# Kernel optimization log

Measured on AMD Instinct MI355X. Metric: run time of the kernel, lower is better.

Reference implementation:

```python
import jax, jax.numpy as jnp
import numpy as np
import math

B, C, A, W, H = 8, 128, 16, 64, 64


def setup_inputs() -> dict:
    key = jax.random.key(0)
    ks = jax.random.split(key, 7)
    s_in = 1.0 / math.sqrt(C)
    return {
        "x": jax.random.normal(ks[0], (B, C, W, H), dtype=jnp.float32),
        "Wq": jax.random.normal(ks[1], (A, C), dtype=jnp.float32) * s_in,
        "bq": jnp.zeros((A,), dtype=jnp.float32),
        "Wk": jax.random.normal(ks[2], (A, C), dtype=jnp.float32) * s_in,
        "bk": jnp.zeros((A,), dtype=jnp.float32),
        "Wv": jax.random.normal(ks[3], (C, C), dtype=jnp.float32) * s_in,
        "bv": jnp.zeros((C,), dtype=jnp.float32),
    }


def reference(x, Wq, bq, Wk, bk, Wv, bv):
    # 1x1 convs == per-pixel linear projections
    q = jnp.einsum('ac,bcwh->bawh', Wq, x) + bq[None, :, None, None]  # [B,A,W,H]
    k = jnp.einsum('ac,bcwh->bawh', Wk, x) + bk[None, :, None, None]  # [B,A,W,H]
    v = jnp.einsum('vc,bcwh->bvwh', Wv, x) + bv[None, :, None, None]  # [B,C,W,H]

    scale = 1.0 / math.sqrt(q.shape[1])
    # full spatial attention: [B, W, H, W, H]
    attn = jnp.einsum('bawh,baWH->bwhWH', q, k)
    b, w, h, _, _ = attn.shape
    attn = jax.nn.softmax(attn.reshape(b, w, h, -1) * scale, axis=-1)
    attn = attn.reshape(b, w, h, w, h)
    out = jnp.einsum('bwhWH,bvWH->bvwh', attn, v)  # [B,C,W,H]
    return out
```

## Files before the change

### kernel.cpp

```cpp
#include <hip/hip_runtime.h>
#include <math.h>

#define BB 8
#define CC 128
#define NN 4096

typedef _Float16 f16;
typedef _Float16 f16x4v __attribute__((ext_vector_type(4)));
typedef _Float16 f16x8 __attribute__((ext_vector_type(8)));
typedef float f32x4v __attribute__((ext_vector_type(4)));
typedef float f32x16 __attribute__((ext_vector_type(16)));

#if __has_builtin(__builtin_amdgcn_exp2f)
#define EXP2(x) __builtin_amdgcn_exp2f(x)
#else
#define EXP2(x) __expf((x)*0.69314718056f)
#endif

#define QSCALE 0.360673760222f
#define SHIFT  5.770780163555f

#define WF_BYTES 65536

__global__ __launch_bounds__(256)
void prep_kernel(const float* __restrict__ Wq, const float* __restrict__ bq,
                 const float* __restrict__ Wk, const float* __restrict__ bk,
                 const float* __restrict__ Wv, const float* __restrict__ bv,
                 f16* __restrict__ Wf, float* __restrict__ biasS)
{
    const int tg = blockIdx.x*256 + threadIdx.x;
    if (tg < 2560) {
        const int mt = tg >> 9, ks = (tg >> 6) & 7, l = tg & 63;
        const int n32 = l & 31, h = l >> 5;
        const int r = mt*32 + n32;
        f16x8 v8;
        #pragma unroll
        for (int i = 0; i < 8; i++) {
            int c = ks*16 + 8*h + i;
            float wv_;
            if (r < 16)      wv_ = QSCALE * Wq[r*CC + c];
            else if (r < 32) wv_ = Wk[(r-16)*CC + c];
            else             wv_ = Wv[(r-32)*CC + c];
            v8[i] = (f16)wv_;
        }
        *(f16x8*)&Wf[(size_t)tg*8] = v8;
    }
    if (blockIdx.x == 0 && threadIdx.x < 160) {
        int r = threadIdx.x;
        biasS[r] = r < 16 ? QSCALE*bq[r] : (r < 32 ? bk[r-16] : bv[r-32]);
    }
}

__global__ __launch_bounds__(256)
void proj_kernel(const float* __restrict__ x, const f16* __restrict__ Wf,
                 const float* __restrict__ biasS,
                 f16* __restrict__ Qt, f16* __restrict__ Kt, f16* __restrict__ Vf)
{
    __shared__ __align__(16) f16 Vl[CC*140];

    const int tid  = threadIdx.x;
    const int lane = tid & 63;
    const int wv   = tid >> 6;
    const int b    = blockIdx.x & 7;
    const int pt   = blockIdx.x >> 3;
    const int n32  = lane & 31;
    const int half = lane >> 5;
    const int p    = pt*128 + wv*32 + n32;

    const float* xp = x + (size_t)b*CC*NN + p;
    f16x8 xf[8];
    #pragma unroll
    for (int ks = 0; ks < 8; ks++) {
        float xv[8];
        #pragma unroll
        for (int i = 0; i < 8; i++)
            xv[i] = __builtin_nontemporal_load(&xp[(size_t)(ks*16 + 8*half + i)*NN]);
        #pragma unroll
        for (int i = 0; i < 8; i++) xf[ks][i] = (f16)xv[i];
    }

    f32x16 acc[5];
    #pragma unroll
    for (int mt = 0; mt < 5; mt++) acc[mt] = (f32x16)0.0f;
    #pragma unroll
    for (int ks = 0; ks < 8; ks++) {
        #pragma unroll
        for (int mt = 0; mt < 5; mt++) {
            f16x8 wfr = *(const f16x8*)&Wf[((size_t)(mt*8 + ks)*64 + lane)*8];
            acc[mt] = __builtin_amdgcn_mfma_f32_32x32x16_f16(wfr, xf[ks], acc[mt], 0, 0, 0);
        }
    }

    #pragma unroll
    for (int mt = 0; mt < 5; mt++) {
        #pragma unroll
        for (int q = 0; q < 4; q++) {
            float4 b4 = *(const float4*)&biasS[mt*32 + q*8 + 4*half];
            acc[mt][q*4+0] += b4.x; acc[mt][q*4+1] += b4.y;
            acc[mt][q*4+2] += b4.z; acc[mt][q*4+3] += b4.w;
        }
    }

    {
        size_t qkoff = ((size_t)b*NN + p)*16;
        f16x4v s0, s1, s2, s3;
        #pragma unroll
        for (int i = 0; i < 4; i++) {
            s0[i] = (f16)acc[0][i];    s1[i] = (f16)acc[0][4+i];
            s2[i] = (f16)acc[0][8+i];  s3[i] = (f16)acc[0][12+i];
        }
        *(f16x4v*)&Qt[qkoff + 4*half]     = s0;
        *(f16x4v*)&Qt[qkoff + 8 + 4*half] = s1;
        *(f16x4v*)&Kt[qkoff + 4*half]     = s2;
        *(f16x4v*)&Kt[qkoff + 8 + 4*half] = s3;
    }

    #pragma unroll
    for (int mt = 1; mt < 5; mt++) {
        #pragma unroll
        for (int g = 0; g < 16; g++) {
            int c = (mt-1)*32 + (g & 3) + 8*(g >> 2) + 4*half;
            Vl[c*140 + wv*32 + n32] = (f16)acc[mt][g];
        }
    }
    __syncthreads();

    #pragma unroll
    for (int pass = 0; pass < 8; pass++) {
        int item = pass*256 + tid;
        int l    = item & 63;
        int f    = (item >> 6) & 15;
        int ktl  = item >> 10;
        int c16  = f >> 2, ct = f & 3;
        int li   = l & 31, h2 = l >> 5;
        const f16* src = &Vl[(ct*32 + li)*140 + ktl*64 + c16*16 + 4*h2];
        f16x4v lo = *(const f16x4v*)&src[0];
        f16x4v hi = *(const f16x4v*)&src[8];
        f16x8 v8;
        #pragma unroll
        for (int i = 0; i < 4; i++) { v8[i] = lo[i]; v8[4+i] = hi[i]; }
        int ktg = pt*2 + ktl;
        *(f16x8*)&Vf[((((size_t)b*64 + ktg)*16 + c16*4 + ct)*64 + l)*8] = v8;
    }
}

__global__ __launch_bounds__(256, 2)
void attn_kernel(const f16* __restrict__ Qt, const f16* __restrict__ Kt,
                 const f16* __restrict__ Vf, float* __restrict__ out)
{
    __shared__ __align__(16) unsigned char lds_raw[27776];

    const int tid  = threadIdx.x;
    const int lane = tid & 63;
    const int wv   = tid >> 6;
    const int b    = blockIdx.x & 7;
    const int qt   = blockIdx.x >> 3;
    const int q0   = qt*32;
    const int n32  = lane & 31;
    const int half = lane >> 5;

    const f16* vb = Vf + (size_t)b*64*16*512;
    const f16* kb = Kt + (size_t)b*NN*16;
    const f16x8 qf = *(const f16x8*)&Qt[((size_t)b*NN + q0 + n32)*16 + half*8];

    f32x16 of[4];
    #pragma unroll
    for (int ct = 0; ct < 4; ct++) of[ct] = (f32x16)0.0f;
    float ps[4] = {0.f, 0.f, 0.f, 0.f};

    f16x8 kf0 = *(const f16x8*)&kb[((size_t)wv*64 + n32)*16 + half*8];
    f16x8 kf1 = *(const f16x8*)&kb[((size_t)wv*64 + 32 + n32)*16 + half*8];
    f16x8 vpf[16];
    {
        const f16* vt = vb + (size_t)wv*8192;
        #pragma unroll
        for (int i = 0; i < 16; i++)
            vpf[i] = *(const f16x8*)&vt[((size_t)i*64 + lane)*8];
    }

    for (int kt = wv; kt < NN/64; kt += 4) {
        const int ktn = (kt + 4 < NN/64) ? kt + 4 : kt;
        f16x8 kf0n = *(const f16x8*)&kb[((size_t)ktn*64 + n32)*16 + half*8];
        f16x8 kf1n = *(const f16x8*)&kb[((size_t)ktn*64 + 32 + n32)*16 + half*8];

        f32x16 St0 = __builtin_amdgcn_mfma_f32_32x32x16_f16(kf0, qf, (f32x16)(-SHIFT), 0, 0, 0);
        f32x16 St1 = __builtin_amdgcn_mfma_f32_32x32x16_f16(kf1, qf, (f32x16)(-SHIFT), 0, 0, 0);

        f16x8 pf[4];
        #pragma unroll
        for (int g = 0; g < 16; g++) {
            float e0 = EXP2(St0[g]); ps[g & 3] += e0; pf[(g >> 3)][g & 7]     = (f16)e0;
            float e1 = EXP2(St1[g]); ps[g & 3] += e1; pf[2 + (g >> 3)][g & 7] = (f16)e1;
        }

        const f16* vtn = vb + (size_t)ktn*8192;
        #pragma unroll
        for (int kc = 0; kc < 4; kc++) {
            #pragma unroll
            for (int ct = 0; ct < 4; ct++) {
                const int i = kc*4 + ct;
                f16x8 vc = vpf[i];
                vpf[i] = *(const f16x8*)&vtn[((size_t)i*64 + lane)*8];
                of[ct] = __builtin_amdgcn_mfma_f32_32x32x16_f16(pf[kc], vc, of[ct], 0, 0, 0);
            }
        }
        kf0 = kf0n; kf1 = kf1n;
    }

    float ls = (ps[0] + ps[1]) + (ps[2] + ps[3]);
    ls += __shfl_xor(ls, 32);

    __syncthreads();
    if (wv != 0) {
        unsigned char* base = lds_raw + (size_t)(wv-1)*9216 + (size_t)lane*144;
        #pragma unroll
        for (int ct = 0; ct < 4; ct++) {
            #pragma unroll
            for (int h = 0; h < 2; h++) {
                f16x8 t;
                #pragma unroll
                for (int jj = 0; jj < 8; jj++) t[jj] = (f16)of[ct][h*8+jj];
                *(f16x8*)(base + ct*32 + h*16) = t;
            }
        }
        *(float*)(base + 128) = ls;
    }
    __syncthreads();
    if (wv == 0) {
        #pragma unroll
        for (int s2 = 0; s2 < 3; s2++) {
            unsigned char* base = lds_raw + (size_t)s2*9216 + (size_t)lane*144;
            #pragma unroll
            for (int ct = 0; ct < 4; ct++) {
                #pragma unroll
                for (int h = 0; h < 2; h++) {
                    f16x8 t = *(const f16x8*)(base + ct*32 + h*16);
                    #pragma unroll
                    for (int jj = 0; jj < 8; jj++) of[ct][h*8+jj] += (float)t[jj];
                }
            }
            ls += *(const float*)(base + 128);
        }
        float* ls_inv = (float*)(lds_raw + 27648);
        if (lane < 32) ls_inv[lane] = 1.f / ls;
        float invq[16];
        #pragma unroll
        for (int g = 0; g < 16; g++)
            invq[g] = ls_inv[(g & 3) + 8*(g >> 2) + 4*half];
        float* Tb = (float*)lds_raw;
        #pragma unroll
        for (int ct = 0; ct < 4; ct++) {
            #pragma unroll
            for (int g = 0; g < 16; g++) {
                int row = (g & 3) + 8*(g >> 2) + 4*half;
                Tb[(ct*32 + n32)*36 + row] = of[ct][g] * invq[g];
            }
        }
    }
    __syncthreads();
    {
        const float* Tb = (const float*)lds_raw;
        #pragma unroll
        for (int it = 0; it < 4; it++) {
            int idx = it*256 + tid;
            int c = idx >> 3, qq = idx & 7;
            f32x4v v = *(const f32x4v*)&Tb[c*36 + qq*4];
            __builtin_nontemporal_store(v,
                (f32x4v*)&out[((size_t)b*CC + c)*NN + q0 + qq*4]);
        }
    }
}

extern "C" void kernel_launch(void* const* d_in, const int* in_sizes, int n_in,
                              void* d_out, int out_size, void* d_ws, size_t ws_size,
                              hipStream_t stream) {
    const float* x  = (const float*)d_in[0];
    const float* Wq = (const float*)d_in[1];
    const float* bq = (const float*)d_in[2];
    const float* Wk = (const float*)d_in[3];
    const float* bk = (const float*)d_in[4];
    const float* Wv = (const float*)d_in[5];
    const float* bv = (const float*)d_in[6];
    float* out = (float*)d_out;

    f16* Qw = (f16*)d_ws;
    f16* Kw = Qw + (size_t)BB*NN*16;
    f16* Vw = Kw + (size_t)BB*NN*16;
    unsigned char* tail = (unsigned char*)d_out + (size_t)out_size*4 - WF_BYTES;
    f16*   Wf    = (f16*)tail;
    float* biasS = (float*)(tail + 49152);

    hipLaunchKernelGGL(prep_kernel, dim3(10), dim3(256), 0, stream,
                       Wq, bq, Wk, bk, Wv, bv, Wf, biasS);
    hipLaunchKernelGGL(proj_kernel, dim3(256), dim3(256), 0, stream,
                       x, Wf, biasS, Qw, Kw, Vw);
    hipLaunchKernelGGL(attn_kernel, dim3(1024), dim3(256), 0, stream,
                       Qw, Kw, Vw, out);
}
```

Baseline: 136.7 us.

## Process 64 queries per block with waves split over channel pairs and key halves

```diff
diff --git a/kernel.cpp b/kernel.cpp
--- a/kernel.cpp
+++ b/kernel.cpp
@@ -148,125 +148,163 @@
 void attn_kernel(const f16* __restrict__ Qt, const f16* __restrict__ Kt,
                  const f16* __restrict__ Vf, float* __restrict__ out)
 {
-    __shared__ __align__(16) unsigned char lds_raw[27776];
+    __shared__ __align__(16) unsigned char lds_raw[53504];
 
     const int tid  = threadIdx.x;
     const int lane = tid & 63;
     const int wv   = tid >> 6;
+    const int cp   = wv & 1;
+    const int kh   = wv >> 1;
     const int b    = blockIdx.x & 7;
     const int qt   = blockIdx.x >> 3;
-    const int q0   = qt*32;
+    const int q0   = qt*64;
     const int n32  = lane & 31;
     const int half = lane >> 5;
 
     const f16* vb = Vf + (size_t)b*64*16*512;
     const f16* kb = Kt + (size_t)b*NN*16;
-    const f16x8 qf = *(const f16x8*)&Qt[((size_t)b*NN + q0 + n32)*16 + half*8];
-
-    f32x16 of[4];
-    #pragma unroll
-    for (int ct = 0; ct < 4; ct++) of[ct] = (f32x16)0.0f;
-    float ps[4] = {0.f, 0.f, 0.f, 0.f};
-
-    f16x8 kf0 = *(const f16x8*)&kb[((size_t)wv*64 + n32)*16 + half*8];
-    f16x8 kf1 = *(const f16x8*)&kb[((size_t)wv*64 + 32 + n32)*16 + half*8];
-    f16x8 vpf[16];
+    const f16x8 qfA = *(const f16x8*)&Qt[((size_t)b*NN + q0 + n32)*16 + half*8];
+    const f16x8 qfB = *(const f16x8*)&Qt[((size_t)b*NN + q0 + 32 + n32)*16 + half*8];
+
+    f32x16 ofA[2], ofB[2];
+    #pragma unroll
+    for (int c = 0; c < 2; c++) { ofA[c] = (f32x16)0.0f; ofB[c] = (f32x16)0.0f; }
+    float psA[4] = {0.f, 0.f, 0.f, 0.f};
+    float psB[4] = {0.f, 0.f, 0.f, 0.f};
+
+    f16x8 kf0 = *(const f16x8*)&kb[((size_t)kh*64 + n32)*16 + half*8];
+    f16x8 kf1 = *(const f16x8*)&kb[((size_t)kh*64 + 32 + n32)*16 + half*8];
+    f16x8 vpf[8];
     {
-        const f16* vt = vb + (size_t)wv*8192;
-        #pragma unroll
-        for (int i = 0; i < 16; i++)
-            vpf[i] = *(const f16x8*)&vt[((size_t)i*64 + lane)*8];
-    }
-
-    for (int kt = wv; kt < NN/64; kt += 4) {
-        const int ktn = (kt + 4 < NN/64) ? kt + 4 : kt;
+        const f16* vt = vb + (size_t)kh*8192;
+        #pragma unroll
+        for (int kc = 0; kc < 4; kc++)
+            #pragma unroll
+            for (int j = 0; j < 2; j++)
+                vpf[kc*2+j] = *(const f16x8*)&vt[((size_t)(kc*4 + 2*cp + j)*64 + lane)*8];
+    }
+
+    for (int kt = kh; kt < NN/64; kt += 2) {
+        const int ktn = (kt + 2 < NN/64) ? kt + 2 : kt;
         f16x8 kf0n = *(const f16x8*)&kb[((size_t)ktn*64 + n32)*16 + half*8];
         f16x8 kf1n = *(const f16x8*)&kb[((size_t)ktn*64 + 32 + n32)*16 + half*8];
 
-        f32x16 St0 = __builtin_amdgcn_mfma_f32_32x32x16_f16(kf0, qf, (f32x16)(-SHIFT), 0, 0, 0);
-        f32x16 St1 = __builtin_amdgcn_mfma_f32_32x32x16_f16(kf1, qf, (f32x16)(-SHIFT), 0, 0, 0);
-
-        f16x8 pf[4];
-        #pragma unroll
-        for (int g = 0; g < 16; g++) {
-            float e0 = EXP2(St0[g]); ps[g & 3] += e0; pf[(g >> 3)][g & 7]     = (f16)e0;
-            float e1 = EXP2(St1[g]); ps[g & 3] += e1; pf[2 + (g >> 3)][g & 7] = (f16)e1;
+        f16x8 pfA[4];
+        {
+            f32x16 St0 = __builtin_amdgcn_mfma_f32_32x32x16_f16(kf0, qfA, (f32x16)(-SHIFT), 0, 0, 0);
+            f32x16 St1 = __builtin_amdgcn_mfma_f32_32x32x16_f16(kf1, qfA, (f32x16)(-SHIFT), 0, 0, 0);
+            #pragma unroll
+            for (int g = 0; g < 16; g++) {
+                float e0 = EXP2(St0[g]); psA[g & 3] += e0; pfA[(g >> 3)][g & 7]     = (f16)e0;
+                float e1 = EXP2(St1[g]); psA[g & 3] += e1; pfA[2 + (g >> 3)][g & 7] = (f16)e1;
+            }
+        }
+        f16x8 pfB[4];
+        {
+            f32x16 St0 = __builtin_amdgcn_mfma_f32_32x32x16_f16(kf0, qfB, (f32x16)(-SHIFT), 0, 0, 0);
+            f32x16 St1 = __builtin_amdgcn_mfma_f32_32x32x16_f16(kf1, qfB, (f32x16)(-SHIFT), 0, 0, 0);
+            #pragma unroll
+            for (int g = 0; g < 16; g++) {
+                float e0 = EXP2(St0[g]); psB[g & 3] += e0; pfB[(g >> 3)][g & 7]     = (f16)e0;
+                float e1 = EXP2(St1[g]); psB[g & 3] += e1; pfB[2 + (g >> 3)][g & 7] = (f16)e1;
+            }
         }
 
         const f16* vtn = vb + (size_t)ktn*8192;
         #pragma unroll
         for (int kc = 0; kc < 4; kc++) {
             #pragma unroll
-            for (int ct = 0; ct < 4; ct++) {
-                const int i = kc*4 + ct;
-                f16x8 vc = vpf[i];
-                vpf[i] = *(const f16x8*)&vtn[((size_t)i*64 + lane)*8];
-                of[ct] = __builtin_amdgcn_mfma_f32_32x32x16_f16(pf[kc], vc, of[ct], 0, 0, 0);
+            for (int j = 0; j < 2; j++) {
+                const int ii = kc*2 + j;
+                f16x8 vc = vpf[ii];
+                vpf[ii] = *(const f16x8*)&vtn[((size_t)(kc*4 + 2*cp + j)*64 + lane)*8];
+                ofA[j] = __builtin_amdgcn_mfma_f32_32x32x16_f16(pfA[kc], vc, ofA[j], 0, 0, 0);
+                ofB[j] = __builtin_amdgcn_mfma_f32_32x32x16_f16(pfB[kc], vc, ofB[j], 0, 0, 0);
             }
         }
         kf0 = kf0n; kf1 = kf1n;
     }
 
-    float ls = (ps[0] + ps[1]) + (ps[2] + ps[3]);
-    ls += __shfl_xor(ls, 32);
-
-    __syncthreads();
-    if (wv != 0) {
-        unsigned char* base = lds_raw + (size_t)(wv-1)*9216 + (size_t)lane*144;
-        #pragma unroll
-        for (int ct = 0; ct < 4; ct++) {
+    float lsA = (psA[0] + psA[1]) + (psA[2] + psA[3]);
+    lsA += __shfl_xor(lsA, 32);
+    float lsB = (psB[0] + psB[1]) + (psB[2] + psB[3]);
+    lsB += __shfl_xor(lsB, 32);
+
+    __syncthreads();
+    if (wv >= 2) {
+        unsigned char* base = lds_raw + (size_t)cp*9216 + (size_t)lane*144;
+        #pragma unroll
+        for (int a = 0; a < 4; a++) {
             #pragma unroll
             for (int h = 0; h < 2; h++) {
                 f16x8 t;
                 #pragma unroll
-                for (int jj = 0; jj < 8; jj++) t[jj] = (f16)of[ct][h*8+jj];
-                *(f16x8*)(base + ct*32 + h*16) = t;
-            }
-        }
-        *(float*)(base + 128) = ls;
-    }
-    __syncthreads();
-    if (wv == 0) {
-        #pragma unroll
-        for (int s2 = 0; s2 < 3; s2++) {
-            unsigned char* base = lds_raw + (size_t)s2*9216 + (size_t)lane*144;
-            #pragma unroll
-            for (int ct = 0; ct < 4; ct++) {
+                for (int jj = 0; jj < 8; jj++)
+                    t[jj] = (f16)((a < 2 ? ofA[a & 1] : ofB[a & 1])[h*8 + jj]);
+                *(f16x8*)(base + a*32 + h*16) = t;
+            }
+        }
+        *(float*)(base + 128) = lsA;
+        *(float*)(base + 132) = lsB;
+    }
+    __syncthreads();
+    if (wv < 2) {
+        unsigned char* base = lds_raw + (size_t)cp*9216 + (size_t)lane*144;
+        #pragma unroll
+        for (int a = 0; a < 4; a++) {
+            #pragma unroll
+            for (int h = 0; h < 2; h++) {
+                f16x8 t = *(const f16x8*)(base + a*32 + h*16);
                 #pragma unroll
-                for (int h = 0; h < 2; h++) {
-                    f16x8 t = *(const f16x8*)(base + ct*32 + h*16);
+                for (int jj = 0; jj < 8; jj++) {
+                    float v = (float)t[jj];
+                    if (a < 2) ofA[a & 1][h*8 + jj] += v;
+                    else       ofB[a & 1][h*8 + jj] += v;
+                }
+            }
+        }
+        if (wv == 0) {
+            float lsA2 = *(const float*)(base + 128);
+            float lsB2 = *(const float*)(base + 132);
+            float* ls_inv = (float*)(lds_raw + 18432);
+            if (lane < 32) {
+                ls_inv[n32]      = 1.f / (lsA + lsA2);
+                ls_inv[32 + n32] = 1.f / (lsB + lsB2);
+            }
+        }
+    }
+    __syncthreads();
+
+    if (wv < 2) {
+        const float* ls_inv = (const float*)(lds_raw + 18432);
+        float* Tb = (float*)(lds_raw + 18688);
+        #pragma unroll
+        for (int qts = 0; qts < 2; qts++) {
+            #pragma unroll
+            for (int j = 0; j < 4; j++) {
+                f32x4v iv = *(const f32x4v*)&ls_inv[qts*32 + 8*j + 4*half];
+                #pragma unroll
+                for (int ctl = 0; ctl < 2; ctl++) {
+                    const int c = (2*cp + ctl)*32 + n32;
+                    f32x4v o;
                     #pragma unroll
-                    for (int jj = 0; jj < 8; jj++) of[ct][h*8+jj] += (float)t[jj];
+                    for (int e = 0; e < 4; e++)
+                        o[e] = (qts ? ofB[ctl] : ofA[ctl])[4*j + e] * iv[e];
+                    *(f32x4v*)&Tb[(size_t)c*68 + qts*32 + 8*j + 4*half] = o;
                 }
             }
-            ls += *(const float*)(base + 128);
-        }
-        float* ls_inv = (float*)(lds_raw + 27648);
-        if (lane < 32) ls_inv[lane] = 1.f / ls;
-        float invq[16];
-        #pragma unroll
-        for (int g = 0; g < 16; g++)
-            invq[g] = ls_inv[(g & 3) + 8*(g >> 2) + 4*half];
-        float* Tb = (float*)lds_raw;
-        #pragma unroll
-        for (int ct = 0; ct < 4; ct++) {
-            #pragma unroll
-            for (int g = 0; g < 16; g++) {
-                int row = (g & 3) + 8*(g >> 2) + 4*half;
-                Tb[(ct*32 + n32)*36 + row] = of[ct][g] * invq[g];
-            }
         }
     }
     __syncthreads();
     {
-        const float* Tb = (const float*)lds_raw;
-        #pragma unroll
-        for (int it = 0; it < 4; it++) {
+        const float* Tb = (const float*)(lds_raw + 18688);
+        #pragma unroll
+        for (int it = 0; it < 8; it++) {
             int idx = it*256 + tid;
-            int c = idx >> 3, qq = idx & 7;
-            f32x4v v = *(const f32x4v*)&Tb[c*36 + qq*4];
+            int c = idx >> 4, qg = idx & 15;
+            f32x4v v = *(const f32x4v*)&Tb[(size_t)c*68 + qg*4];
             __builtin_nontemporal_store(v,
-                (f32x4v*)&out[((size_t)b*CC + c)*NN + q0 + qq*4]);
+                (f32x4v*)&out[((size_t)b*CC + c)*NN + q0 + qg*4]);
         }
     }
 }
@@ -294,6 +332,6 @@
                        Wq, bq, Wk, bk, Wv, bv, Wf, biasS);
     hipLaunchKernelGGL(proj_kernel, dim3(256), dim3(256), 0, stream,
                        x, Wf, biasS, Qw, Kw, Vw);
-    hipLaunchKernelGGL(attn_kernel, dim3(1024), dim3(256), 0, stream,
+    hipLaunchKernelGGL(attn_kernel, dim3(512), dim3(256), 0, stream,
                        Qw, Kw, Vw, out);
 }
```

Result: no change. 139.1 us (+1.7%).

## Split attention work across waves by channel tile with LDS-shared probabilities

Applied to the files above, without the earlier changes.

```diff
diff --git a/kernel.cpp b/kernel.cpp
--- a/kernel.cpp
+++ b/kernel.cpp
@@ -6,15 +6,26 @@
 #define NN 4096
 
 typedef _Float16 f16;
+typedef _Float16 f16x2 __attribute__((ext_vector_type(2)));
 typedef _Float16 f16x4v __attribute__((ext_vector_type(4)));
 typedef _Float16 f16x8 __attribute__((ext_vector_type(8)));
 typedef float f32x4v __attribute__((ext_vector_type(4)));
 typedef float f32x16 __attribute__((ext_vector_type(16)));
+typedef int i32x4 __attribute__((ext_vector_type(4)));
 
 #if __has_builtin(__builtin_amdgcn_exp2f)
 #define EXP2(x) __builtin_amdgcn_exp2f(x)
 #else
 #define EXP2(x) __expf((x)*0.69314718056f)
+#endif
+
+#if __has_builtin(__builtin_amdgcn_cvt_pkrtz) && __has_builtin(__builtin_amdgcn_fdot2)
+#define CVTPK(a,b)    __builtin_amdgcn_cvt_pkrtz((a),(b))
+#define FDOT2(pk,acc) __builtin_amdgcn_fdot2((pk), one2_, (acc), false)
+#else
+static __device__ inline f16x2 cvtpk_fb(float a, float b){ f16x2 r; r[0]=(f16)a; r[1]=(f16)b; return r; }
+#define CVTPK(a,b)    cvtpk_fb((a),(b))
+#define FDOT2(pk,acc) ((acc) + (float)(pk)[0] + (float)(pk)[1])
 #endif
 
 #define QSCALE 0.360673760222f
@@ -144,130 +155,129 @@
     }
 }
 
-__global__ __launch_bounds__(256, 2)
+__global__ __launch_bounds__(256, 4)
 void attn_kernel(const f16* __restrict__ Qt, const f16* __restrict__ Kt,
                  const f16* __restrict__ Vf, float* __restrict__ out)
 {
-    __shared__ __align__(16) unsigned char lds_raw[27776];
+    __shared__ __align__(16) unsigned char lds_raw[19072];
 
     const int tid  = threadIdx.x;
     const int lane = tid & 63;
-    const int wv   = tid >> 6;
+    const int w    = tid >> 6;
     const int b    = blockIdx.x & 7;
     const int qt   = blockIdx.x >> 3;
     const int q0   = qt*32;
     const int n32  = lane & 31;
     const int half = lane >> 5;
+    const int myhalf = w & 1;
+    const int mypar  = w >> 1;
 
     const f16* vb = Vf + (size_t)b*64*16*512;
     const f16* kb = Kt + (size_t)b*NN*16;
     const f16x8 qf = *(const f16x8*)&Qt[((size_t)b*NN + q0 + n32)*16 + half*8];
 
-    f32x16 of[4];
-    #pragma unroll
-    for (int ct = 0; ct < 4; ct++) of[ct] = (f32x16)0.0f;
-    float ps[4] = {0.f, 0.f, 0.f, 0.f};
-
-    f16x8 kf0 = *(const f16x8*)&kb[((size_t)wv*64 + n32)*16 + half*8];
-    f16x8 kf1 = *(const f16x8*)&kb[((size_t)wv*64 + 32 + n32)*16 + half*8];
-    f16x8 vpf[16];
+    f16* Pex = (f16*)lds_raw;
+    const auto one2_ = CVTPK(1.0f, 1.0f);
+
+    f32x16 of = (f32x16)0.0f;
+    float ls = 0.0f;
+
+    f16x8 kf = *(const f16x8*)&kb[((size_t)(mypar*64 + myhalf*32 + n32))*16 + half*8];
+    f16x8 vpf[4];
+    #pragma unroll
+    for (int kc = 0; kc < 4; kc++)
+        vpf[kc] = *(const f16x8*)&vb[((size_t)(kc*4 + w)*64 + lane)*8];
+
+#define PROD(ST, PAR)                                                          \
+    {                                                                          \
+        i32x4 lo_, hi_;                                                        \
+        _Pragma("unroll")                                                      \
+        for (int e = 0; e < 8; e++) {                                          \
+            float ea_ = EXP2((ST)[2*e]);                                       \
+            float eb_ = EXP2((ST)[2*e+1]);                                     \
+            auto pk_ = CVTPK(ea_, eb_);                                        \
+            ls = FDOT2(pk_, ls);                                               \
+            if (e < 4) lo_[e]   = __builtin_bit_cast(int, pk_);                \
+            else       hi_[e-4] = __builtin_bit_cast(int, pk_);                \
+        }                                                                      \
+        f16* wr_ = &Pex[((size_t)((PAR)*4 + 2*myhalf)*64 + lane)*8];           \
+        *(i32x4*)&wr_[0]   = lo_;                                              \
+        *(i32x4*)&wr_[512] = hi_;                                              \
+    }
+
+    for (int kt2 = 0; kt2 < 64; kt2 += 2) {
+        if (w < 2) {
+            f32x16 St = __builtin_amdgcn_mfma_f32_32x32x16_f16(kf, qf, (f32x16)(-SHIFT), 0, 0, 0);
+            {
+                const int tn = (kt2 + 2 < 64) ? kt2 + 2 : kt2;
+                kf = *(const f16x8*)&kb[((size_t)(tn*64 + myhalf*32 + n32))*16 + half*8];
+            }
+            PROD(St, 0)
+        }
+        asm volatile("s_waitcnt lgkmcnt(0)\n\ts_barrier" ::: "memory");
+        {
+            const f16* vtn = vb + (size_t)(kt2 + 1)*8192;
+            #pragma unroll
+            for (int kc = 0; kc < 4; kc++) {
+                f16x8 pq = *(const f16x8*)&Pex[((size_t)kc*64 + lane)*8];
+                f16x8 vc = vpf[kc];
+                vpf[kc] = *(const f16x8*)&vtn[((size_t)(kc*4 + w)*64 + lane)*8];
+                of = __builtin_amdgcn_mfma_f32_32x32x16_f16(pq, vc, of, 0, 0, 0);
+            }
+        }
+        if (w >= 2) {
+            f32x16 St = __builtin_amdgcn_mfma_f32_32x32x16_f16(kf, qf, (f32x16)(-SHIFT), 0, 0, 0);
+            {
+                const int tn = (kt2 + 3 < 64) ? kt2 + 3 : kt2 + 1;
+                kf = *(const f16x8*)&kb[((size_t)(tn*64 + myhalf*32 + n32))*16 + half*8];
+            }
+            PROD(St, 1)
+        }
+        asm volatile("s_waitcnt lgkmcnt(0)\n\ts_barrier" ::: "memory");
+        {
+            const int tv = (kt2 + 2 < 64) ? kt2 + 2 : 63;
+            const f16* vtn = vb + (size_t)tv*8192;
+            #pragma unroll
+            for (int kc = 0; kc < 4; kc++) {
+                f16x8 pq = *(const f16x8*)&Pex[((size_t)(4 + kc)*64 + lane)*8];
+                f16x8 vc = vpf[kc];
+                vpf[kc] = *(const f16x8*)&vtn[((size_t)(kc*4 + w)*64 + lane)*8];
+                of = __builtin_amdgcn_mfma_f32_32x32x16_f16(pq, vc, of, 0, 0, 0);
+            }
+        }
+    }
+#undef PROD
+
+    float ls2 = ls + __shfl_xor(ls, 32);
+    __syncthreads();
+    float* ls_part = (float*)(lds_raw + 18432);
+    float* ls_inv  = (float*)(lds_raw + 18944);
+    if (lane < 32) ls_part[w*32 + n32] = ls2;
+    __syncthreads();
+    if (w == 0 && lane < 32)
+        ls_inv[n32] = 1.0f / (ls_part[n32] + ls_part[32 + n32] +
+                              ls_part[64 + n32] + ls_part[96 + n32]);
+    __syncthreads();
+    float* Tb = (float*)lds_raw;
     {
-        const f16* vt = vb + (size_t)wv*8192;
-        #pragma unroll
-        for (int i = 0; i < 16; i++)
-            vpf[i] = *(const f16x8*)&vt[((size_t)i*64 + lane)*8];
-    }
-
-    for (int kt = wv; kt < NN/64; kt += 4) {
-        const int ktn = (kt + 4 < NN/64) ? kt + 4 : kt;
-        f16x8 kf0n = *(const f16x8*)&kb[((size_t)ktn*64 + n32)*16 + half*8];
-        f16x8 kf1n = *(const f16x8*)&kb[((size_t)ktn*64 + 32 + n32)*16 + half*8];
-
-        f32x16 St0 = __builtin_amdgcn_mfma_f32_32x32x16_f16(kf0, qf, (f32x16)(-SHIFT), 0, 0, 0);
-        f32x16 St1 = __builtin_amdgcn_mfma_f32_32x32x16_f16(kf1, qf, (f32x16)(-SHIFT), 0, 0, 0);
-
-        f16x8 pf[4];
+        f32x4v iv[4];
+        #pragma unroll
+        for (int t = 0; t < 4; t++)
+            iv[t] = *(const f32x4v*)&ls_inv[t*8 + 4*half];
         #pragma unroll
         for (int g = 0; g < 16; g++) {
-            float e0 = EXP2(St0[g]); ps[g & 3] += e0; pf[(g >> 3)][g & 7]     = (f16)e0;
-            float e1 = EXP2(St1[g]); ps[g & 3] += e1; pf[2 + (g >> 3)][g & 7] = (f16)e1;
-        }
-
-        const f16* vtn = vb + (size_t)ktn*8192;
-        #pragma unroll
-        for (int kc = 0; kc < 4; kc++) {
-            #pragma unroll
-            for (int ct = 0; ct < 4; ct++) {
-                const int i = kc*4 + ct;
-                f16x8 vc = vpf[i];
-                vpf[i] = *(const f16x8*)&vtn[((size_t)i*64 + lane)*8];
-                of[ct] = __builtin_amdgcn_mfma_f32_32x32x16_f16(pf[kc], vc, of[ct], 0, 0, 0);
-            }
-        }
-        kf0 = kf0n; kf1 = kf1n;
-    }
-
-    float ls = (ps[0] + ps[1]) + (ps[2] + ps[3]);
-    ls += __shfl_xor(ls, 32);
-
-    __syncthreads();
-    if (wv != 0) {
-        unsigned char* base = lds_raw + (size_t)(wv-1)*9216 + (size_t)lane*144;
-        #pragma unroll
-        for (int ct = 0; ct < 4; ct++) {
-            #pragma unroll
-            for (int h = 0; h < 2; h++) {
-                f16x8 t;
-                #pragma unroll
-                for (int jj = 0; jj < 8; jj++) t[jj] = (f16)of[ct][h*8+jj];
-                *(f16x8*)(base + ct*32 + h*16) = t;
-            }
-        }
-        *(float*)(base + 128) = ls;
-    }
-    __syncthreads();
-    if (wv == 0) {
-        #pragma unroll
-        for (int s2 = 0; s2 < 3; s2++) {
-            unsigned char* base = lds_raw + (size_t)s2*9216 + (size_t)lane*144;
-            #pragma unroll
-            for (int ct = 0; ct < 4; ct++) {
-                #pragma unroll
-                for (int h = 0; h < 2; h++) {
-                    f16x8 t = *(const f16x8*)(base + ct*32 + h*16);
-                    #pragma unroll
-                    for (int jj = 0; jj < 8; jj++) of[ct][h*8+jj] += (float)t[jj];
-                }
-            }
-            ls += *(const float*)(base + 128);
-        }
-        float* ls_inv = (float*)(lds_raw + 27648);
-        if (lane < 32) ls_inv[lane] = 1.f / ls;
-        float invq[16];
-        #pragma unroll
-        for (int g = 0; g < 16; g++)
-            invq[g] = ls_inv[(g & 3) + 8*(g >> 2) + 4*half];
-        float* Tb = (float*)lds_raw;
-        #pragma unroll
-        for (int ct = 0; ct < 4; ct++) {
-            #pragma unroll
-            for (int g = 0; g < 16; g++) {
-                int row = (g & 3) + 8*(g >> 2) + 4*half;
-                Tb[(ct*32 + n32)*36 + row] = of[ct][g] * invq[g];
-            }
-        }
-    }
-    __syncthreads();
-    {
-        const float* Tb = (const float*)lds_raw;
-        #pragma unroll
-        for (int it = 0; it < 4; it++) {
-            int idx = it*256 + tid;
-            int c = idx >> 3, qq = idx & 7;
-            f32x4v v = *(const f32x4v*)&Tb[c*36 + qq*4];
-            __builtin_nontemporal_store(v,
-                (f32x4v*)&out[((size_t)b*CC + c)*NN + q0 + qq*4]);
-        }
+            int row = (g & 3) + 8*(g >> 2) + 4*half;
+            Tb[(size_t)(w*32 + n32)*36 + row] = of[g] * iv[g >> 2][g & 3];
+        }
+    }
+    __syncthreads();
+    #pragma unroll
+    for (int it = 0; it < 4; it++) {
+        int idx = it*256 + tid;
+        int c = idx >> 3, qg = idx & 7;
+        f32x4v v = *(const f32x4v*)&Tb[(size_t)c*36 + qg*4];
+        __builtin_nontemporal_store(v,
+            (f32x4v*)&out[((size_t)b*CC + c)*NN + q0 + qg*4]);
     }
 }
 
```

Measured after the change: 144.6 us. 5.8% more time.

## Share LDS-staged V tiles across waves with 64-query blocks and split channels

Applied to the files above, without the earlier changes.

```diff
diff --git a/kernel.cpp b/kernel.cpp
--- a/kernel.cpp
+++ b/kernel.cpp
@@ -148,112 +148,111 @@
 void attn_kernel(const f16* __restrict__ Qt, const f16* __restrict__ Kt,
                  const f16* __restrict__ Vf, float* __restrict__ out)
 {
-    __shared__ __align__(16) unsigned char lds_raw[27776];
+    __shared__ __align__(16) unsigned char lds_raw[65536];
 
     const int tid  = threadIdx.x;
     const int lane = tid & 63;
-    const int wv   = tid >> 6;
+    const int w    = tid >> 6;
+    const int qp   = w & 1;
+    const int pw   = w >> 1;
     const int b    = blockIdx.x & 7;
     const int qt   = blockIdx.x >> 3;
-    const int q0   = qt*32;
+    const int q0   = qt*64;
     const int n32  = lane & 31;
     const int half = lane >> 5;
 
     const f16* vb = Vf + (size_t)b*64*16*512;
     const f16* kb = Kt + (size_t)b*NN*16;
-    const f16x8 qf = *(const f16x8*)&Qt[((size_t)b*NN + q0 + n32)*16 + half*8];
-
-    f32x16 of[4];
-    #pragma unroll
-    for (int ct = 0; ct < 4; ct++) of[ct] = (f32x16)0.0f;
+    const f16x8 qf = *(const f16x8*)&Qt[((size_t)b*NN + q0 + qp*32 + n32)*16 + half*8];
+
+    f32x16 of0 = (f32x16)0.0f, of1 = (f32x16)0.0f;
     float ps[4] = {0.f, 0.f, 0.f, 0.f};
 
-    f16x8 kf0 = *(const f16x8*)&kb[((size_t)wv*64 + n32)*16 + half*8];
-    f16x8 kf1 = *(const f16x8*)&kb[((size_t)wv*64 + 32 + n32)*16 + half*8];
-    f16x8 vpf[16];
-    {
-        const f16* vt = vb + (size_t)wv*8192;
-        #pragma unroll
-        for (int i = 0; i < 16; i++)
-            vpf[i] = *(const f16x8*)&vt[((size_t)i*64 + lane)*8];
-    }
-
-    for (int kt = wv; kt < NN/64; kt += 4) {
-        const int ktn = (kt + 4 < NN/64) ? kt + 4 : kt;
-        f16x8 kf0n = *(const f16x8*)&kb[((size_t)ktn*64 + n32)*16 + half*8];
-        f16x8 kf1n = *(const f16x8*)&kb[((size_t)ktn*64 + 32 + n32)*16 + half*8];
-
-        f32x16 St0 = __builtin_amdgcn_mfma_f32_32x32x16_f16(kf0, qf, (f32x16)(-SHIFT), 0, 0, 0);
-        f32x16 St1 = __builtin_amdgcn_mfma_f32_32x32x16_f16(kf1, qf, (f32x16)(-SHIFT), 0, 0, 0);
-
-        f16x8 pf[4];
-        #pragma unroll
-        for (int g = 0; g < 16; g++) {
-            float e0 = EXP2(St0[g]); ps[g & 3] += e0; pf[(g >> 3)][g & 7]     = (f16)e0;
-            float e1 = EXP2(St1[g]); ps[g & 3] += e1; pf[2 + (g >> 3)][g & 7] = (f16)e1;
-        }
-
-        const f16* vtn = vb + (size_t)ktn*8192;
-        #pragma unroll
-        for (int kc = 0; kc < 4; kc++) {
-            #pragma unroll
-            for (int ct = 0; ct < 4; ct++) {
-                const int i = kc*4 + ct;
-                f16x8 vc = vpf[i];
-                vpf[i] = *(const f16x8*)&vtn[((size_t)i*64 + lane)*8];
-                of[ct] = __builtin_amdgcn_mfma_f32_32x32x16_f16(pf[kc], vc, of[ct], 0, 0, 0);
+    f16* Pb = (f16*)(lds_raw + 49152);
+
+#define STAGE(TILE, BUF)                                                              \
+    {                                                                                 \
+        const unsigned char* gsb = (const unsigned char*)vb + (size_t)(TILE)*16384    \
+                                   + w*4096 + lane*16;                                \
+        unsigned char* lsb = lds_raw + (BUF)*16384 + w*4096;                          \
+        _Pragma("unroll")                                                             \
+        for (int sp = 0; sp < 4; sp++) {                                              \
+            __builtin_amdgcn_global_load_lds(                                         \
+                (const __attribute__((address_space(1))) unsigned int*)(gsb + sp*1024), \
+                (__attribute__((address_space(3))) unsigned int*)(lsb + sp*1024),     \
+                16, 0, 0);                                                            \
+        }                                                                             \
+    }
+
+    STAGE(0, 0)
+    f16x8 kf0 = *(const f16x8*)&kb[((size_t)pw*64 + n32)*16 + half*8];
+    f16x8 kf1 = *(const f16x8*)&kb[((size_t)pw*64 + 32 + n32)*16 + half*8];
+    STAGE(1, 1)
+
+    int vbuf = 0;
+    for (int kt = 0; kt < 64; ++kt) {
+        const int cur = kt & 1;
+        if (cur == pw) {
+            f32x16 St0 = __builtin_amdgcn_mfma_f32_32x32x16_f16(kf0, qf, (f32x16)(-SHIFT), 0, 0, 0);
+            f32x16 St1 = __builtin_amdgcn_mfma_f32_32x32x16_f16(kf1, qf, (f32x16)(-SHIFT), 0, 0, 0);
+            int tl = kt + 2; if (tl > 63) tl = kt;
+            kf0 = *(const f16x8*)&kb[((size_t)tl*64 + n32)*16 + half*8];
+            kf1 = *(const f16x8*)&kb[((size_t)tl*64 + 32 + n32)*16 + half*8];
+            f16x8 po[4];
+            #pragma unroll
+            for (int g = 0; g < 16; g++) {
+                float e0 = EXP2(St0[g]); ps[g & 3] += e0; po[(g >> 3)][g & 7]     = (f16)e0;
+                float e1 = EXP2(St1[g]); ps[g & 3] += e1; po[2 + (g >> 3)][g & 7] = (f16)e1;
             }
-        }
-        kf0 = kf0n; kf1 = kf1n;
-    }
+            f16* wr = Pb + ((size_t)(cur*2 + qp)*4*64 + lane)*8;
+            #pragma unroll
+            for (int kc = 0; kc < 4; kc++)
+                *(f16x8*)&wr[kc*512] = po[kc];
+        }
+        asm volatile("s_waitcnt vmcnt(6) lgkmcnt(0)\n\ts_barrier" ::: "memory");
+        {
+            int tl = kt + 2; if (tl > 63) tl = 63;
+            int sb = vbuf + 2; if (sb >= 3) sb -= 3;
+            STAGE(tl, sb)
+        }
+        {
+            const f16* Vt = (const f16*)lds_raw + (size_t)vbuf*8192;
+            const f16* Pc = Pb + (size_t)cur*4096;
+            #pragma unroll
+            for (int kc = 0; kc < 4; kc++) {
+                f16x8 vc = *(const f16x8*)&Vt[((size_t)(kc*4 + w)*64 + lane)*8];
+                f16x8 p0 = *(const f16x8*)&Pc[((size_t)kc*64 + lane)*8];
+                f16x8 p1 = *(const f16x8*)&Pc[((size_t)(4 + kc)*64 + lane)*8];
+                of0 = __builtin_amdgcn_mfma_f32_32x32x16_f16(p0, vc, of0, 0, 0, 0);
+                of1 = __builtin_amdgcn_mfma_f32_32x32x16_f16(p1, vc, of1, 0, 0, 0);
+            }
+        }
+        vbuf = (vbuf + 1 == 3) ? 0 : vbuf + 1;
+    }
+#undef STAGE
 
     float ls = (ps[0] + ps[1]) + (ps[2] + ps[3]);
     ls += __shfl_xor(ls, 32);
-
-    __syncthreads();
-    if (wv != 0) {
-        unsigned char* base = lds_raw + (size_t)(wv-1)*9216 + (size_t)lane*144;
-        #pragma unroll
-        for (int ct = 0; ct < 4; ct++) {
-            #pragma unroll
-            for (int h = 0; h < 2; h++) {
-                f16x8 t;
+    __syncthreads();
+    float* ls_part = (float*)(lds_raw + 49152);
+    float* ls_inv  = (float*)(lds_raw + 49664);
+    if (lane < 32) ls_part[w*32 + n32] = ls;
+    __syncthreads();
+    if (w < 2 && lane < 32)
+        ls_inv[w*32 + n32] = 1.0f / (ls_part[w*32 + n32] + ls_part[(w+2)*32 + n32]);
+    __syncthreads();
+    {
+        float* Tb = (float*)lds_raw;
+        #pragma unroll
+        for (int qs = 0; qs < 2; qs++) {
+            #pragma unroll
+            for (int j = 0; j < 4; j++) {
+                f32x4v iv = *(const f32x4v*)&ls_inv[qs*32 + 8*j + 4*half];
+                f32x4v o;
                 #pragma unroll
-                for (int jj = 0; jj < 8; jj++) t[jj] = (f16)of[ct][h*8+jj];
-                *(f16x8*)(base + ct*32 + h*16) = t;
-            }
-        }
-        *(float*)(base + 128) = ls;
-    }
-    __syncthreads();
-    if (wv == 0) {
-        #pragma unroll
-        for (int s2 = 0; s2 < 3; s2++) {
-            unsigned char* base = lds_raw + (size_t)s2*9216 + (size_t)lane*144;
-            #pragma unroll
-            for (int ct = 0; ct < 4; ct++) {
-                #pragma unroll
-                for (int h = 0; h < 2; h++) {
-                    f16x8 t = *(const f16x8*)(base + ct*32 + h*16);
-                    #pragma unroll
-                    for (int jj = 0; jj < 8; jj++) of[ct][h*8+jj] += (float)t[jj];
-                }
-            }
-            ls += *(const float*)(base + 128);
-        }
-        float* ls_inv = (float*)(lds_raw + 27648);
-        if (lane < 32) ls_inv[lane] = 1.f / ls;
-        float invq[16];
-        #pragma unroll
-        for (int g = 0; g < 16; g++)
-            invq[g] = ls_inv[(g & 3) + 8*(g >> 2) + 4*half];
-        float* Tb = (float*)lds_raw;
-        #pragma unroll
-        for (int ct = 0; ct < 4; ct++) {
-            #pragma unroll
-            for (int g = 0; g < 16; g++) {
-                int row = (g & 3) + 8*(g >> 2) + 4*half;
-                Tb[(ct*32 + n32)*36 + row] = of[ct][g] * invq[g];
+                for (int e = 0; e < 4; e++)
+                    o[e] = (qs ? of1 : of0)[4*j + e] * iv[e];
+                *(f32x4v*)&Tb[(size_t)(w*32 + n32)*68 + qs*32 + 8*j + 4*half] = o;
             }
         }
     }
@@ -261,12 +260,12 @@
     {
         const float* Tb = (const float*)lds_raw;
         #pragma unroll
-        for (int it = 0; it < 4; it++) {
+        for (int it = 0; it < 8; it++) {
             int idx = it*256 + tid;
-            int c = idx >> 3, qq = idx & 7;
-            f32x4v v = *(const f32x4v*)&Tb[c*36 + qq*4];
+            int c = idx >> 4, qg = idx & 15;
+            f32x4v v = *(const f32x4v*)&Tb[(size_t)c*68 + qg*4];
             __builtin_nontemporal_store(v,
-                (f32x4v*)&out[((size_t)b*CC + c)*NN + q0 + qq*4]);
+                (f32x4v*)&out[((size_t)b*CC + c)*NN + q0 + qg*4]);
         }
     }
 }
@@ -294,6 +293,6 @@
                        Wq, bq, Wk, bk, Wv, bv, Wf, biasS);
     hipLaunchKernelGGL(proj_kernel, dim3(256), dim3(256), 0, stream,
                        x, Wf, biasS, Qw, Kw, Vw);
-    hipLaunchKernelGGL(attn_kernel, dim3(1024), dim3(256), 0, stream,
+    hipLaunchKernelGGL(attn_kernel, dim3(512), dim3(256), 0, stream,
                        Qw, Kw, Vw, out);
 }
```

Measured after the change: 148.8 us. 8.8% more time.
